# Optimization experiments

Hardware: AMD Instinct MI355X
Metric: run time of the kernel (lower is better)

Reference implementation:

```python
import jax, jax.numpy as jnp
import numpy as np

BLK = 128          # block size for fp8 block-wise scales
FP8_MAX = 448.0    # max representable magnitude of float8_e4m3fn


def _dequant_act(a, s):
    # a: (E, M, K) fp8 values stored in fp32; s: (E, M, K//BLK) per-token 1x128 scales
    E, M, K = a.shape
    nb = K // BLK
    return (a.reshape(E, M, nb, BLK) * s[..., None]).reshape(E, M, K)


def _dequant_w(w, s):
    # w: (E, N, K) fp8 values stored in fp32; s: (E, N//BLK, K//BLK) 128x128 block scales
    E, N, K = w.shape
    return (w.reshape(E, N // BLK, BLK, K // BLK, BLK) * s[:, :, None, :, None]).reshape(E, N, K)


def _fp8_round(x):
    # round-to-fp8(e4m3fn) with straight-through value semantics
    q = x.astype(jnp.float8_e4m3fn).astype(jnp.float32)
    return x + jax.lax.stop_gradient(q - x)


def setup_inputs() -> dict:
    key = jax.random.key(0)
    ks = jax.random.split(key, 8)
    E, N, K, M = 8, 2048, 4096, 1024
    f8 = lambda x: x.astype(jnp.float8_e4m3fn).astype(jnp.float32)
    hidden_states_fp8 = f8(jax.random.normal(ks[0], (E, M, K), dtype=jnp.float32))
    hidden_states_scale = jax.random.uniform(ks[1], (E, M, K // BLK), dtype=jnp.float32, minval=0.01, maxval=1.0)
    masked_m = jax.random.randint(ks[2], (E,), 1, M + 1, dtype=jnp.int32)
    w13_weight_fp8 = f8(jax.random.normal(ks[3], (E, N, K), dtype=jnp.float32))
    w13_weight_scale = jax.random.uniform(ks[4], (E, N // BLK, K // BLK), dtype=jnp.float32, minval=0.01, maxval=1.0)
    w2_weight_fp8 = f8(jax.random.normal(ks[5], (E, K, N // 2), dtype=jnp.float32))
    w2_weight_scale = jax.random.uniform(ks[6], (E, K // BLK, N // 2 // BLK), dtype=jnp.float32, minval=0.01, maxval=1.0)
    return {
        "hidden_states_fp8": hidden_states_fp8,
        "hidden_states_scale": hidden_states_scale,
        "masked_m": masked_m,
        "expected_m": 512,
        "w13_weight_fp8": w13_weight_fp8,
        "w13_weight_scale": w13_weight_scale,
        "w2_weight_fp8": w2_weight_fp8,
        "w2_weight_scale": w2_weight_scale,
    }


def reference(hidden_states_fp8, hidden_states_scale, masked_m, expected_m,
              w13_weight_fp8, w13_weight_scale, w2_weight_fp8, w2_weight_scale):
    E, M, K = hidden_states_fp8.shape
    # per-expert row validity mask (rows >= masked_m[e] are padding)
    mask = jnp.arange(M)[None, :] < masked_m[:, None]            # (E, M)

    # --- grouped GEMM 1: (x @ w13^T) -> bf16, masked by valid rows ---
    a = _dequant_act(hidden_states_fp8, hidden_states_scale)     # (E, M, K)
    w13 = _dequant_w(w13_weight_fp8, w13_weight_scale)           # (E, N, K)
    gateup = jnp.einsum('emk,enk->emn', a, w13)
    gateup = gateup.astype(jnp.bfloat16).astype(jnp.float32)     # gemm emits bf16

    # --- fused SiLU * mul + per-128-block fp8 quantization ---
    gate, up = jnp.split(gateup, 2, axis=-1)                     # (E, M, N/2) each
    x = jax.nn.silu(gate) * up
    x = jnp.where(mask[..., None], x, 0.0)
    N2 = x.shape[-1]
    nb = N2 // BLK
    xb = x.reshape(E, M, nb, BLK)
    amax = jnp.max(jnp.abs(xb), axis=-1)                         # (E, M, nb)
    scale = jnp.maximum(amax, 1e-10) / FP8_MAX
    q = _fp8_round(xb / scale[..., None])                        # fp8-rounded values
    a2 = (q * scale[..., None]).reshape(E, M, N2)                # dequantized for gemm 2

    # --- grouped GEMM 2: (down_input @ w2^T) -> bf16 ---
    w2 = _dequant_w(w2_weight_fp8, w2_weight_scale)              # (E, K, N/2)
    out = jnp.einsum('emn,ekn->emk', a2, w2).astype(jnp.bfloat16)
    out = jnp.where(mask[..., None], out, jnp.bfloat16(0))
    return out
```

## Files before the change

kernel.cpp:

```cpp
#include <hip/hip_runtime.h>
#include <hip/hip_bf16.h>

#define E_  8
#define M_  1024
#define K_  4096
#define N_  2048
#define N2_ 1024

typedef unsigned short u16;
typedef unsigned int   u32;

typedef __bf16 bf16x8 __attribute__((ext_vector_type(8)));
typedef float  f32x4  __attribute__((ext_vector_type(4)));

union FragU { uint4 u; bf16x8 v; };

__device__ __forceinline__ u16 f2bfu(float f){
  union { __hip_bfloat16 h; u16 u; } c;
  c.h = __float2bfloat16(f);
  return c.u;
}
__device__ __forceinline__ u32 pack2(float a, float b){
  return (u32)f2bfu(a) | ((u32)f2bfu(b) << 16);
}
__device__ __forceinline__ float bf2f(u16 u){
  u32 x = ((u32)u) << 16;
  return __uint_as_float(x);
}
__device__ __forceinline__ float bf16val(float f){
  return bf2f(f2bfu(f));
}
__device__ __forceinline__ float fp8_round(float x){
  float ax = fabsf(x);
  if (ax < 0.015625f){
    return rintf(x * 512.0f) * (1.0f/512.0f);
  }
  u32 u = __float_as_uint(x);
  u32 lsb = (u >> 20) & 1u;
  u += 0x7FFFFu + lsb;
  u &= 0xFFF00000u;
  return __uint_as_float(u);
}

#define GLD16(g, l) __builtin_amdgcn_global_load_lds( \
    (const __attribute__((address_space(1))) void*)(g), \
    (__attribute__((address_space(3))) void*)(l), 16, 0, 0)

__global__ __launch_bounds__(512) void conv_hs_kernel(
    const float* __restrict__ hs, const float* __restrict__ hss,
    const int* __restrict__ masked_m, u16* __restrict__ hs16)
{
  const int m = blockIdx.x, e = blockIdx.y;
  if (m >= masked_m[e]) return;
  const int c = threadIdx.x;
  const float s = hss[((size_t)e*M_ + m)*(K_/128) + (c >> 4)];
  const float* src = hs + ((size_t)e*M_ + m)*K_ + c*8;
  const float4 f0 = *reinterpret_cast<const float4*>(src);
  const float4 f1 = *reinterpret_cast<const float4*>(src + 4);
  uint4 w;
  w.x = pack2(f0.x * s, f0.y * s);
  w.y = pack2(f0.z * s, f0.w * s);
  w.z = pack2(f1.x * s, f1.y * s);
  w.w = pack2(f1.z * s, f1.w * s);
  const int cd = (c & ~7) | ((c & 7) ^ (m & 7));
  *reinterpret_cast<uint4*>(hs16 + ((size_t)e*M_ + m)*K_ + cd*8) = w;
}

template<int AMODE, int KD, int ND>
__global__ __launch_bounds__(256, 2) void gemm_grouped(
    const u16* __restrict__ Abf, const float* __restrict__ Bptr,
    const float* __restrict__ Wscale, const int* __restrict__ masked_m,
    void* __restrict__ Cout)
{
  constexpr int BK  = 64;
  constexpr int KT  = KD / BK;
  constexpr int NKB = KD / 128;
  const int tn = blockIdx.x, tm = blockIdx.y, e = blockIdx.z;
  const int m0 = tm * 128, n0 = tn * 128;
  const int me = masked_m[e];
  const int tid = threadIdx.x;

  u16*   const Cu = (u16*)Cout;
  float* const Cf = (float*)Cout;

  if (m0 >= me){
    if constexpr (AMODE == 1){
      const uint4 z = make_uint4(0u,0u,0u,0u);
      #pragma unroll
      for (int q = 0; q < 16; ++q){
        int idx = tid + 256*q;
        int r = idx >> 5, c = idx & 31;
        *reinterpret_cast<uint4*>(Cf + ((size_t)e*M_ + m0 + r)*ND + n0 + c*4) = z;
      }
    }
    return;
  }

  __shared__ u16 sA[2][128*64];
  __shared__ u16 sB[2][128*64];

  const int lane = tid & 63, wid = tid >> 6;
  const int rrow = tid >> 3;
  const int kq   = tid & 7;

  float4 rB[8];
  float  sWv = 0.f;

  auto ISSUE_A = [&](int kt, int buf){
    const int k0 = kt * BK;
    #pragma unroll
    for (int q = 0; q < 4; ++q){
      const int ins = wid*4 + q;
      const int r   = ins*8 + (lane >> 3);
      const u16* src = Abf + ((size_t)e*M_ + m0 + r)*KD + k0 + (lane & 7)*8;
      GLD16(src, &sA[buf][ins*512]);
    }
  };

  auto LOAD_B = [&](int kt){
    const int k0 = kt * BK;
    const int kb = k0 >> 7;
    sWv = Wscale[((size_t)e*(ND/128) + tn)*NKB + kb];
    #pragma unroll
    for (int p = 0; p < 4; ++p){
      const int r = p*32 + rrow;
      const float* bp = Bptr + ((size_t)e*ND + n0 + r)*KD + k0 + kq*8;
      rB[2*p]   = *reinterpret_cast<const float4*>(bp);
      rB[2*p+1] = *reinterpret_cast<const float4*>(bp + 4);
    }
  };

  auto WRITE_B = [&](int buf){
    #pragma unroll
    for (int p = 0; p < 4; ++p){
      const int r   = p*32 + rrow;
      const int dst = r*64 + ((kq ^ (r & 7)) * 8);
      uint4 wb;
      wb.x = pack2(rB[2*p].x * sWv,   rB[2*p].y * sWv);
      wb.y = pack2(rB[2*p].z * sWv,   rB[2*p].w * sWv);
      wb.z = pack2(rB[2*p+1].x * sWv, rB[2*p+1].y * sWv);
      wb.w = pack2(rB[2*p+1].z * sWv, rB[2*p+1].w * sWv);
      *reinterpret_cast<uint4*>(&sB[buf][dst]) = wb;
    }
  };

  const int wm = wid >> 1, wn = wid & 1;
  const int fr = lane & 15, kg = lane >> 4;

  f32x4 acc[4][4];
  #pragma unroll
  for (int i = 0; i < 4; ++i)
    #pragma unroll
    for (int j = 0; j < 4; ++j)
      acc[i][j] = (f32x4){0.f, 0.f, 0.f, 0.f};

  auto COMPUTE = [&](int buf){
    #pragma unroll
    for (int ks = 0; ks < 2; ++ks){
      FragU av[4], bv[4];
      #pragma unroll
      for (int i = 0; i < 4; ++i){
        const int r  = wm*64 + i*16 + fr;
        const int ch = (ks*4 + kg) ^ (r & 7);
        av[i].u = *reinterpret_cast<const uint4*>(&sA[buf][r*64 + ch*8]);
      }
      #pragma unroll
      for (int j = 0; j < 4; ++j){
        const int r  = wn*64 + j*16 + fr;
        const int ch = (ks*4 + kg) ^ (r & 7);
        bv[j].u = *reinterpret_cast<const uint4*>(&sB[buf][r*64 + ch*8]);
      }
      #pragma unroll
      for (int i = 0; i < 4; ++i)
        #pragma unroll
        for (int j = 0; j < 4; ++j)
          acc[i][j] = __builtin_amdgcn_mfma_f32_16x16x32_bf16(av[i].v, bv[j].v, acc[i][j], 0, 0, 0);
    }
  };

  ISSUE_A(0, 0);
  LOAD_B(0);
  WRITE_B(0);
  __syncthreads();
  int cur = 0;
  for (int kt = 0; kt < KT; ++kt){
    if (kt + 1 < KT){
      ISSUE_A(kt + 1, cur ^ 1);
      LOAD_B(kt + 1);
    }
    COMPUTE(cur);
    if (kt + 1 < KT) WRITE_B(cur ^ 1);
    __syncthreads();
    cur ^= 1;
  }

  #pragma unroll
  for (int i = 0; i < 4; ++i){
    #pragma unroll
    for (int j = 0; j < 4; ++j){
      #pragma unroll
      for (int r = 0; r < 4; ++r){
        const int gm = m0 + wm*64 + i*16 + kg*4 + r;
        const int gn = n0 + wn*64 + j*16 + fr;
        if constexpr (AMODE == 0){
          if (gm < me) Cu[((size_t)e*M_ + gm)*ND + gn] = f2bfu(acc[i][j][r]);
        } else {
          const float v = (gm < me) ? bf16val(acc[i][j][r]) : 0.0f;
          Cf[((size_t)e*M_ + gm)*ND + gn] = v;
        }
      }
    }
  }
}

__global__ __launch_bounds__(128) void act_quant_kernel(
    const u16* __restrict__ gu, const int* __restrict__ masked_m,
    u16* __restrict__ a2)
{
  const int m = blockIdx.x, e = blockIdx.y;
  if (m >= masked_m[e]) return;
  const int t = threadIdx.x;
  const u16* row = gu + ((size_t)e*M_ + m)*N_;
  uint4 g4 = *reinterpret_cast<const uint4*>(row + t*8);
  uint4 u4 = *reinterpret_cast<const uint4*>(row + N2_ + t*8);
  u32 gp[4] = {g4.x, g4.y, g4.z, g4.w};
  u32 up[4] = {u4.x, u4.y, u4.z, u4.w};

  float x[8];
  #pragma unroll
  for (int w = 0; w < 4; ++w){
    float g0 = bf2f((u16)(gp[w] & 0xffffu));
    float g1 = bf2f((u16)(gp[w] >> 16));
    float u0 = bf2f((u16)(up[w] & 0xffffu));
    float u1 = bf2f((u16)(up[w] >> 16));
    x[2*w]   = g0 / (1.0f + expf(-g0)) * u0;
    x[2*w+1] = g1 / (1.0f + expf(-g1)) * u1;
  }

  float amax = 0.f;
  #pragma unroll
  for (int k = 0; k < 8; ++k) amax = fmaxf(amax, fabsf(x[k]));
  #pragma unroll
  for (int o = 8; o > 0; o >>= 1) amax = fmaxf(amax, __shfl_xor(amax, o, 16));
  const float scale = fmaxf(amax, 1e-10f) / 448.0f;

  u32 hh[4];
  #pragma unroll
  for (int w = 0; w < 4; ++w){
    float d0 = fp8_round(x[2*w]   / scale) * scale;
    float d1 = fp8_round(x[2*w+1] / scale) * scale;
    hh[w] = pack2(d0, d1);
  }
  uint4 o4 = make_uint4(hh[0], hh[1], hh[2], hh[3]);
  const int td = (t & ~7) | ((t & 7) ^ (m & 7));
  *reinterpret_cast<uint4*>(a2 + ((size_t)e*M_ + m)*N2_ + td*8) = o4;
}

extern "C" void kernel_launch(void* const* d_in, const int* in_sizes, int n_in,
                              void* d_out, int out_size, void* d_ws, size_t ws_size,
                              hipStream_t stream)
{
  const float* hs   = (const float*)d_in[0];
  const float* hss  = (const float*)d_in[1];
  const int*   mm   = (const int*)d_in[2];
  const float* w13  = (const float*)d_in[4];
  const float* w13s = (const float*)d_in[5];
  const float* w2   = (const float*)d_in[6];
  const float* w2s  = (const float*)d_in[7];

  u16* gu   = (u16*)d_out;
  u16* hs16 = (u16*)d_out + (size_t)E_*M_*N_;
  u16* a2   = (u16*)d_ws;

  conv_hs_kernel<<<dim3(M_, E_), dim3(512), 0, stream>>>(hs, hss, mm, hs16);
  gemm_grouped<0, K_, N_><<<dim3(N_/128, M_/128, E_), dim3(256), 0, stream>>>(
      hs16, w13, w13s, mm, gu);
  act_quant_kernel<<<dim3(M_, E_), dim3(128), 0, stream>>>(gu, mm, a2);
  gemm_grouped<1, N2_, K_><<<dim3(K_/128, M_/128, E_), dim3(256), 0, stream>>>(
      a2, w2, w2s, mm, d_out);
}
```

Before: 331.6 us.

## Run first grouped GEMM in fp8 MFMA with per-block scale application

Packs the fp8-valued fp32 activations and w13 weights into real 8-bit storage with a new conversion kernel, then runs GEMM1 on fp8 MFMA instructions. The 128x128 weight scale and per-row activation scale are applied to each K-block's partial accumulator instead of dequantizing operands before the multiply. This halves operand bytes in shared memory and global traffic and uses the higher-rate fp8 matrix path. In exchange the whole w13 tensor must be converted on every call, a separate pass over fp32 weights plus extra scratch writes into the output buffer.

```diff
diff --git a/kernel.cpp b/kernel.cpp
--- a/kernel.cpp
+++ b/kernel.cpp
@@ -8,7 +8,9 @@
 #define N2_ 1024
 
 typedef unsigned short u16;
+typedef unsigned char  u8;
 typedef unsigned int   u32;
+typedef long           i64;
 
 typedef __bf16 bf16x8 __attribute__((ext_vector_type(8)));
 typedef float  f32x4  __attribute__((ext_vector_type(4)));
@@ -41,36 +43,159 @@
   u &= 0xFFF00000u;
   return __uint_as_float(u);
 }
+__device__ __forceinline__ u32 f2fp8(float v){
+  u32 b = __float_as_uint(v);
+  u32 s = (b >> 24) & 0x80u;
+  int e = (int)((b >> 23) & 0xffu);
+  u32 m = (b >> 20) & 7u;
+  if (e >= 121) return s | ((u32)(e - 120) << 3) | m;
+  return s | (u32)(fabsf(v) * 512.0f + 0.25f);
+}
 
 #define GLD16(g, l) __builtin_amdgcn_global_load_lds( \
     (const __attribute__((address_space(1))) void*)(g), \
     (__attribute__((address_space(3))) void*)(l), 16, 0, 0)
 
-__global__ __launch_bounds__(512) void conv_hs_kernel(
-    const float* __restrict__ hs, const float* __restrict__ hss,
-    const int* __restrict__ masked_m, u16* __restrict__ hs16)
-{
-  const int m = blockIdx.x, e = blockIdx.y;
-  if (m >= masked_m[e]) return;
-  const int c = threadIdx.x;
-  const float s = hss[((size_t)e*M_ + m)*(K_/128) + (c >> 4)];
-  const float* src = hs + ((size_t)e*M_ + m)*K_ + c*8;
-  const float4 f0 = *reinterpret_cast<const float4*>(src);
-  const float4 f1 = *reinterpret_cast<const float4*>(src + 4);
+template<bool MASKED>
+__global__ __launch_bounds__(256) void conv8_kernel(
+    const float* __restrict__ src_, const int* __restrict__ masked_m,
+    u8* __restrict__ dst)
+{
+  const int row = blockIdx.x, e = blockIdx.y;
+  if (MASKED && row >= masked_m[e]) return;
+  const int t = threadIdx.x;
+  const size_t R = (size_t)e*gridDim.x + row;
+  const float* s = src_ + R*K_ + t*16;
+  const float4 f0 = *reinterpret_cast<const float4*>(s);
+  const float4 f1 = *reinterpret_cast<const float4*>(s + 4);
+  const float4 f2 = *reinterpret_cast<const float4*>(s + 8);
+  const float4 f3 = *reinterpret_cast<const float4*>(s + 12);
   uint4 w;
-  w.x = pack2(f0.x * s, f0.y * s);
-  w.y = pack2(f0.z * s, f0.w * s);
-  w.z = pack2(f1.x * s, f1.y * s);
-  w.w = pack2(f1.z * s, f1.w * s);
-  const int cd = (c & ~7) | ((c & 7) ^ (m & 7));
-  *reinterpret_cast<uint4*>(hs16 + ((size_t)e*M_ + m)*K_ + cd*8) = w;
-}
-
-template<int AMODE, int KD, int ND>
-__global__ __launch_bounds__(256, 2) void gemm_grouped(
+  w.x = f2fp8(f0.x) | (f2fp8(f0.y)<<8) | (f2fp8(f0.z)<<16) | (f2fp8(f0.w)<<24);
+  w.y = f2fp8(f1.x) | (f2fp8(f1.y)<<8) | (f2fp8(f1.z)<<16) | (f2fp8(f1.w)<<24);
+  w.z = f2fp8(f2.x) | (f2fp8(f2.y)<<8) | (f2fp8(f2.z)<<16) | (f2fp8(f2.w)<<24);
+  w.w = f2fp8(f3.x) | (f2fp8(f3.y)<<8) | (f2fp8(f3.z)<<16) | (f2fp8(f3.w)<<24);
+  const int td = (t & ~7) | ((t & 7) ^ (row & 7));
+  *reinterpret_cast<uint4*>(dst + R*K_ + td*16) = w;
+}
+
+__global__ __launch_bounds__(256, 2) void gemm1_fp8(
+    const u8* __restrict__ A8, const float* __restrict__ Ascale,
+    const u8* __restrict__ B8, const float* __restrict__ Wscale,
+    const int* __restrict__ masked_m, u16* __restrict__ Cu)
+{
+  const int tn = blockIdx.x, tm = blockIdx.y, e = blockIdx.z;
+  const int m0 = tm*128, n0 = tn*128;
+  const int me = masked_m[e];
+  if (m0 >= me) return;
+  const int tid = threadIdx.x;
+  const int lane = tid & 63, wid = tid >> 6;
+
+  __shared__ u8 sA[2][128*128];
+  __shared__ u8 sB[2][128*128];
+  __shared__ float sSa[2][128];
+
+  const size_t rbA = (size_t)e*M_ + m0;
+  const size_t rbB = (size_t)e*N_ + n0;
+
+  auto ISSUE = [&](const u8* G, size_t rowbase, int kt, u8* Sbuf){
+    #pragma unroll
+    for (int q = 0; q < 4; ++q){
+      const int ins = wid*4 + q;
+      const int r   = ins*8 + (lane >> 3);
+      const u8* src = G + (rowbase + r)*K_ + kt*128 + (lane & 7)*16;
+      GLD16(src, Sbuf + ins*1024);
+    }
+  };
+  auto STAGE_SA = [&](int kt, int buf){
+    if (tid < 128) sSa[buf][tid] = Ascale[(rbA + tid)*32 + kt];
+  };
+
+  const int wm = wid >> 1, wn = wid & 1;
+  const int fr = lane & 15, kg = lane >> 4;
+
+  f32x4 acc[4][4];
+  #pragma unroll
+  for (int i = 0; i < 4; ++i)
+    #pragma unroll
+    for (int j = 0; j < 4; ++j)
+      acc[i][j] = (f32x4){0.f, 0.f, 0.f, 0.f};
+
+  auto COMPUTE = [&](int buf, float sw){
+    f32x4 blk[4][4];
+    #pragma unroll
+    for (int ks = 0; ks < 4; ++ks){
+      i64 av[4], bv[4];
+      #pragma unroll
+      for (int i = 0; i < 4; ++i){
+        const int r   = wm*64 + i*16 + fr;
+        const int c16 = ks*2 + (kg >> 1);
+        const int ad  = r*128 + ((c16 ^ (r & 7)) << 4) + ((kg & 1) << 3);
+        av[i] = *reinterpret_cast<const i64*>(&sA[buf][ad]);
+      }
+      #pragma unroll
+      for (int j = 0; j < 4; ++j){
+        const int r   = wn*64 + j*16 + fr;
+        const int c16 = ks*2 + (kg >> 1);
+        const int ad  = r*128 + ((c16 ^ (r & 7)) << 4) + ((kg & 1) << 3);
+        bv[j] = *reinterpret_cast<const i64*>(&sB[buf][ad]);
+      }
+      #pragma unroll
+      for (int i = 0; i < 4; ++i)
+        #pragma unroll
+        for (int j = 0; j < 4; ++j){
+          f32x4 cin = (ks == 0) ? (f32x4){0.f,0.f,0.f,0.f} : blk[i][j];
+          blk[i][j] = __builtin_amdgcn_mfma_f32_16x16x32_fp8_fp8(av[i], bv[j], cin, 0, 0, 0);
+        }
+    }
+    #pragma unroll
+    for (int i = 0; i < 4; ++i){
+      f32x4 sa = *reinterpret_cast<const f32x4*>(&sSa[buf][wm*64 + i*16 + kg*4]);
+      sa *= sw;
+      #pragma unroll
+      for (int j = 0; j < 4; ++j)
+        acc[i][j] += sa * blk[i][j];
+    }
+  };
+
+  float sw = Wscale[((size_t)e*16 + tn)*32 + 0];
+  ISSUE(A8, rbA, 0, sA[0]);
+  ISSUE(B8, rbB, 0, sB[0]);
+  STAGE_SA(0, 0);
+  __syncthreads();
+  int cur = 0;
+  for (int kt = 0; kt < 32; ++kt){
+    float sw_next = 0.f;
+    if (kt + 1 < 32){
+      ISSUE(A8, rbA, kt + 1, sA[cur ^ 1]);
+      ISSUE(B8, rbB, kt + 1, sB[cur ^ 1]);
+      STAGE_SA(kt + 1, cur ^ 1);
+      sw_next = Wscale[((size_t)e*16 + tn)*32 + kt + 1];
+    }
+    COMPUTE(cur, sw);
+    __syncthreads();
+    cur ^= 1; sw = sw_next;
+  }
+
+  #pragma unroll
+  for (int i = 0; i < 4; ++i){
+    #pragma unroll
+    for (int j = 0; j < 4; ++j){
+      #pragma unroll
+      for (int r = 0; r < 4; ++r){
+        const int gm = m0 + wm*64 + i*16 + kg*4 + r;
+        const int gn = n0 + wn*64 + j*16 + fr;
+        if (gm < me) Cu[((size_t)e*M_ + gm)*N_ + gn] = f2bfu(acc[i][j][r]);
+      }
+    }
+  }
+}
+
+template<int KD, int ND>
+__global__ __launch_bounds__(256, 2) void gemm2_bf16(
     const u16* __restrict__ Abf, const float* __restrict__ Bptr,
     const float* __restrict__ Wscale, const int* __restrict__ masked_m,
-    void* __restrict__ Cout)
+    float* __restrict__ Cf)
 {
   constexpr int BK  = 64;
   constexpr int KT  = KD / BK;
@@ -80,18 +205,13 @@
   const int me = masked_m[e];
   const int tid = threadIdx.x;
 
-  u16*   const Cu = (u16*)Cout;
-  float* const Cf = (float*)Cout;
-
   if (m0 >= me){
-    if constexpr (AMODE == 1){
-      const uint4 z = make_uint4(0u,0u,0u,0u);
-      #pragma unroll
-      for (int q = 0; q < 16; ++q){
-        int idx = tid + 256*q;
-        int r = idx >> 5, c = idx & 31;
-        *reinterpret_cast<uint4*>(Cf + ((size_t)e*M_ + m0 + r)*ND + n0 + c*4) = z;
-      }
+    const uint4 z = make_uint4(0u,0u,0u,0u);
+    #pragma unroll
+    for (int q = 0; q < 16; ++q){
+      int idx = tid + 256*q;
+      int r = idx >> 5, c = idx & 31;
+      *reinterpret_cast<uint4*>(Cf + ((size_t)e*M_ + m0 + r)*ND + n0 + c*4) = z;
     }
     return;
   }
@@ -116,7 +236,6 @@
       GLD16(src, &sA[buf][ins*512]);
     }
   };
-
   auto LOAD_B = [&](int kt){
     const int k0 = kt * BK;
     const int kb = k0 >> 7;
@@ -129,7 +248,6 @@
       rB[2*p+1] = *reinterpret_cast<const float4*>(bp + 4);
     }
   };
-
   auto WRITE_B = [&](int buf){
     #pragma unroll
     for (int p = 0; p < 4; ++p){
@@ -202,12 +320,8 @@
       for (int r = 0; r < 4; ++r){
         const int gm = m0 + wm*64 + i*16 + kg*4 + r;
         const int gn = n0 + wn*64 + j*16 + fr;
-        if constexpr (AMODE == 0){
-          if (gm < me) Cu[((size_t)e*M_ + gm)*ND + gn] = f2bfu(acc[i][j][r]);
-        } else {
-          const float v = (gm < me) ? bf16val(acc[i][j][r]) : 0.0f;
-          Cf[((size_t)e*M_ + gm)*ND + gn] = v;
-        }
+        const float v = (gm < me) ? bf16val(acc[i][j][r]) : 0.0f;
+        Cf[((size_t)e*M_ + gm)*ND + gn] = v;
       }
     }
   }
@@ -268,14 +382,16 @@
   const float* w2   = (const float*)d_in[6];
   const float* w2s  = (const float*)d_in[7];
 
-  u16* gu   = (u16*)d_out;
-  u16* hs16 = (u16*)d_out + (size_t)E_*M_*N_;
-  u16* a2   = (u16*)d_ws;
-
-  conv_hs_kernel<<<dim3(M_, E_), dim3(512), 0, stream>>>(hs, hss, mm, hs16);
-  gemm_grouped<0, K_, N_><<<dim3(N_/128, M_/128, E_), dim3(256), 0, stream>>>(
-      hs16, w13, w13s, mm, gu);
+  u16* gu    = (u16*)d_out;
+  u8*  hs8   = (u8*)d_out + (size_t)E_*M_*N_*2;
+  u8*  w13_8 = (u8*)d_out + (size_t)E_*M_*N_*2 + (size_t)E_*M_*K_;
+  u16* a2    = (u16*)d_ws;
+
+  conv8_kernel<true> <<<dim3(M_, E_), dim3(256), 0, stream>>>(hs,  mm, hs8);
+  conv8_kernel<false><<<dim3(N_, E_), dim3(256), 0, stream>>>(w13, mm, w13_8);
+  gemm1_fp8<<<dim3(N_/128, M_/128, E_), dim3(256), 0, stream>>>(
+      hs8, hss, w13_8, w13s, mm, gu);
   act_quant_kernel<<<dim3(M_, E_), dim3(128), 0, stream>>>(gu, mm, a2);
-  gemm_grouped<1, N2_, K_><<<dim3(K_/128, M_/128, E_), dim3(256), 0, stream>>>(
-      a2, w2, w2s, mm, d_out);
-}
+  gemm2_bf16<N2_, K_><<<dim3(K_/128, M_/128, E_), dim3(256), 0, stream>>>(
+      a2, w2, w2s, mm, (float*)d_out);
+}
```

Result: faster. 293.4 us (-11.5%).
